# Performance work log

Measured on AMD Instinct MI355X. Metric: run time of the kernel, lower is better.

The kernel has to match this reference:

```python
import jax, jax.numpy as jnp
import numpy as np

NUM_NODE_TYPES = 8
HIDDEN = 64
D = 4
N_NODES = 100000
N_EDGES = 3200000
LN_EPS = 1e-5


def setup_inputs() -> dict:
    key = jax.random.key(0)
    ks = jax.random.split(key, 8)
    total_in = 2 * NUM_NODE_TYPES
    out_dim = D * D
    x = jax.random.normal(ks[0], (N_NODES, 16), dtype=jnp.float32)
    edge_index = jax.random.randint(ks[1], (2, N_EDGES), 0, N_NODES, dtype=jnp.int64)
    node_types = jax.random.randint(ks[2], (N_NODES,), 0, NUM_NODE_TYPES, dtype=jnp.int64)
    # LayerNorm params
    ln_g = jnp.ones((total_in,), dtype=jnp.float32)
    ln_b = jnp.zeros((total_in,), dtype=jnp.float32)
    # Linear layers (kaiming-ish init)
    W1 = jax.random.normal(ks[3], (total_in, HIDDEN), dtype=jnp.float32) * (1.0 / np.sqrt(total_in))
    b1 = jnp.zeros((HIDDEN,), dtype=jnp.float32)
    W2 = jax.random.normal(ks[4], (HIDDEN, out_dim), dtype=jnp.float32) * (1.0 / np.sqrt(HIDDEN))
    b2 = jnp.zeros((out_dim,), dtype=jnp.float32)
    return {"x": x, "edge_index": edge_index, "node_types": node_types,
            "ln_g": ln_g, "ln_b": ln_b, "W1": W1, "b1": b1, "W2": W2, "b2": b2}


def reference(x, edge_index, node_types, ln_g, ln_b, W1, b1, W2, b2):
    row, col = edge_index[0], edge_index[1]
    # one-hot node types then per-edge gather of src/tgt types
    onehot = jax.nn.one_hot(node_types, NUM_NODE_TYPES, dtype=jnp.float32)  # [N, T]
    h = jnp.concatenate([onehot[row], onehot[col]], axis=-1)  # [E, 2T]
    # LayerNorm
    mu = jnp.mean(h, axis=-1, keepdims=True)
    var = jnp.mean(jnp.square(h - mu), axis=-1, keepdims=True)
    hn = (h - mu) * jax.lax.rsqrt(var + LN_EPS) * ln_g + ln_b
    # MLP
    h1 = jax.nn.relu(hn @ W1 + b1)          # [E, HIDDEN]
    h_sheaf = (h1 @ W2 + b2).reshape(-1, D, D)  # [E, d, d]
    attention_maps = jax.nn.softmax(h_sheaf, axis=-1)
    sheaf_maps = jnp.eye(D, dtype=h_sheaf.dtype)[None] - attention_maps
    return sheaf_maps
```

## Files before the change

kernel.cpp:

```cpp
#include <hip/hip_runtime.h>
#include <math.h>

#define NUM_T   8
#define TIN     16
#define HID     64
#define OUTD    16
#define LN_EPS  1e-5f

typedef float f32x4 __attribute__((ext_vector_type(4)));

__global__ __launch_bounds__(256) void
build_table_kernel(const float* __restrict__ ln_g,
                   const float* __restrict__ ln_b,
                   const float* __restrict__ W1,
                   const float* __restrict__ b1,
                   const float* __restrict__ W2,
                   const float* __restrict__ b2,
                   f32x4* __restrict__ table4)
{
    __shared__ float sW1[TIN * HID];
    __shared__ float sW2[HID * OUTD];
    __shared__ float sb1[HID];
    __shared__ float sg[TIN], sb[TIN], sb2[OUTD];

    const int t = threadIdx.x;

    for (int i = t; i < TIN * HID; i += 256) sW1[i] = W1[i];
    for (int i = t; i < HID * OUTD; i += 256) sW2[i] = W2[i];
    if (t < HID) sb1[t] = b1[t];
    if (t < TIN) { sg[t] = ln_g[t]; sb[t] = ln_b[t]; }
    if (t < OUTD) sb2[t] = b2[t];
    __syncthreads();

    const int p  = t >> 2;
    const int kg = t & 3;
    const int ts = p >> 3;
    const int tt = p & 7;

    const float mu = 2.0f / 16.0f;
    float var = 0.0f;
    #pragma unroll
    for (int j = 0; j < TIN; ++j) {
        float h = (j == ts || j == (8 + tt)) ? 1.0f : 0.0f;
        float d = h - mu;
        var += d * d;
    }
    var *= (1.0f / 16.0f);
    const float inv = rsqrtf(var + LN_EPS);

    float hn[TIN];
    #pragma unroll
    for (int j = 0; j < TIN; ++j) {
        float h = (j == ts || j == (8 + tt)) ? 1.0f : 0.0f;
        hn[j] = (h - mu) * inv * sg[j] + sb[j];
    }

    float s[OUTD];
    #pragma unroll
    for (int o = 0; o < OUTD; ++o) s[o] = 0.0f;

    const int k0 = kg * 16;
    for (int k = k0; k < k0 + 16; ++k) {
        float a = sb1[k];
        #pragma unroll
        for (int j = 0; j < TIN; ++j) a += hn[j] * sW1[j * HID + k];
        a = fmaxf(a, 0.0f);
        #pragma unroll
        for (int o = 0; o < OUTD; ++o) s[o] += a * sW2[k * OUTD + o];
    }

    #pragma unroll
    for (int o = 0; o < OUTD; ++o) {
        s[o] += __shfl_xor(s[o], 1);
        s[o] += __shfl_xor(s[o], 2);
        s[o] += sb2[o];
    }

    const int r = kg;
    float s0 = s[4*r+0], s1 = s[4*r+1], s2 = s[4*r+2], s3 = s[4*r+3];
    float m  = fmaxf(fmaxf(s0, s1), fmaxf(s2, s3));
    float e0 = expf(s0 - m), e1 = expf(s1 - m),
          e2 = expf(s2 - m), e3 = expf(s3 - m);
    float rs = 1.0f / (e0 + e1 + e2 + e3);
    f32x4 outv;
    outv.x = (r == 0 ? 1.0f : 0.0f) - e0 * rs;
    outv.y = (r == 1 ? 1.0f : 0.0f) - e1 * rs;
    outv.z = (r == 2 ? 1.0f : 0.0f) - e2 * rs;
    outv.w = (r == 3 ? 1.0f : 0.0f) - e3 * rs;

    table4[t] = outv;
}

__global__ __launch_bounds__(256) void
scatter_edges_kernel(const int* __restrict__ row,
                     const int* __restrict__ col,
                     const int* __restrict__ ntypes,
                     const f32x4* __restrict__ table4,
                     f32x4* __restrict__ out4,
                     int E)
{
    __shared__ f32x4 lds_table[64 * 5];
    {
        int p = threadIdx.x >> 2, q = threadIdx.x & 3;
        lds_table[p * 5 + q] = table4[threadIdx.x];
    }
    __syncthreads();

    const int q      = threadIdx.x & 3;
    const int lane_e = threadIdx.x >> 2;
    const int stride = gridDim.x * 64;

    for (int e = blockIdx.x * 64 + lane_e; e < E; e += stride) {
        int r = row[e];
        int c = col[e];
        int pair = ntypes[r] * NUM_T + ntypes[c];
        f32x4 v = lds_table[pair * 5 + q];
        __builtin_nontemporal_store(v, &out4[e * 4 + q]);
    }
}

extern "C" void kernel_launch(void* const* d_in, const int* in_sizes, int n_in,
                              void* d_out, int out_size, void* d_ws, size_t ws_size,
                              hipStream_t stream)
{
    const int*   edge_index = (const int*)d_in[1];
    const int*   ntypes     = (const int*)d_in[2];
    const float* ln_g       = (const float*)d_in[3];
    const float* ln_b       = (const float*)d_in[4];
    const float* W1         = (const float*)d_in[5];
    const float* b1         = (const float*)d_in[6];
    const float* W2         = (const float*)d_in[7];
    const float* b2         = (const float*)d_in[8];

    const int E = in_sizes[1] / 2;

    f32x4* table4 = (f32x4*)d_ws;

    build_table_kernel<<<1, 256, 0, stream>>>(ln_g, ln_b, W1, b1, W2, b2, table4);

    const int blocks = 2048;
    scatter_edges_kernel<<<blocks, 256, 0, stream>>>(
        edge_index, edge_index + E, ntypes,
        table4, (f32x4*)d_out, E);
}
```

Before: 54.09 us.

## Fuse table build into edge kernel and load one index per lane with shuffles

Each of the 2048 blocks now computes the 64-entry sheaf-map table itself in shared memory, which removes the separate single-block launch and its global round trip. The edge loop also changes: each lane loads one edge's row, col and node types, and the pair ids are spread across lanes with wave shuffles. Before, four lanes loaded the same edge indices redundantly. The cost is that every block repeats the small MLP computation and loads the weights into shared memory before it can start scattering.

```diff
diff --git a/kernel.cpp b/kernel.cpp
--- a/kernel.cpp
+++ b/kernel.cpp
@@ -10,18 +10,23 @@
 typedef float f32x4 __attribute__((ext_vector_type(4)));
 
 __global__ __launch_bounds__(256) void
-build_table_kernel(const float* __restrict__ ln_g,
+fused_sheaf_kernel(const int* __restrict__ row,
+                   const int* __restrict__ col,
+                   const int* __restrict__ ntypes,
+                   const float* __restrict__ ln_g,
                    const float* __restrict__ ln_b,
                    const float* __restrict__ W1,
                    const float* __restrict__ b1,
                    const float* __restrict__ W2,
                    const float* __restrict__ b2,
-                   f32x4* __restrict__ table4)
+                   f32x4* __restrict__ out4,
+                   int E)
 {
     __shared__ float sW1[TIN * HID];
     __shared__ float sW2[HID * OUTD];
     __shared__ float sb1[HID];
     __shared__ float sg[TIN], sb[TIN], sb2[OUTD];
+    __shared__ f32x4 lds_table[64 * 5];
 
     const int t = threadIdx.x;
 
@@ -32,90 +37,89 @@
     if (t < OUTD) sb2[t] = b2[t];
     __syncthreads();
 
-    const int p  = t >> 2;
-    const int kg = t & 3;
-    const int ts = p >> 3;
-    const int tt = p & 7;
+    {
+        const int p  = t >> 2;
+        const int kg = t & 3;
+        const int ts = p >> 3;
+        const int tt = p & 7;
 
-    const float mu = 2.0f / 16.0f;
-    float var = 0.0f;
-    #pragma unroll
-    for (int j = 0; j < TIN; ++j) {
-        float h = (j == ts || j == (8 + tt)) ? 1.0f : 0.0f;
-        float d = h - mu;
-        var += d * d;
-    }
-    var *= (1.0f / 16.0f);
-    const float inv = rsqrtf(var + LN_EPS);
+        const float mu = 2.0f / 16.0f;
+        float var = 0.0f;
+        #pragma unroll
+        for (int j = 0; j < TIN; ++j) {
+            float h = (j == ts || j == (8 + tt)) ? 1.0f : 0.0f;
+            float d = h - mu;
+            var += d * d;
+        }
+        var *= (1.0f / 16.0f);
+        const float inv = rsqrtf(var + LN_EPS);
 
-    float hn[TIN];
-    #pragma unroll
-    for (int j = 0; j < TIN; ++j) {
-        float h = (j == ts || j == (8 + tt)) ? 1.0f : 0.0f;
-        hn[j] = (h - mu) * inv * sg[j] + sb[j];
-    }
+        float hn[TIN];
+        #pragma unroll
+        for (int j = 0; j < TIN; ++j) {
+            float h = (j == ts || j == (8 + tt)) ? 1.0f : 0.0f;
+            hn[j] = (h - mu) * inv * sg[j] + sb[j];
+        }
 
-    float s[OUTD];
-    #pragma unroll
-    for (int o = 0; o < OUTD; ++o) s[o] = 0.0f;
+        float s[OUTD];
+        #pragma unroll
+        for (int o = 0; o < OUTD; ++o) s[o] = 0.0f;
 
-    const int k0 = kg * 16;
-    for (int k = k0; k < k0 + 16; ++k) {
-        float a = sb1[k];
+        const int k0 = kg * 16;
+        for (int k = k0; k < k0 + 16; ++k) {
+            float a = sb1[k];
+            #pragma unroll
+            for (int j = 0; j < TIN; ++j) a += hn[j] * sW1[j * HID + k];
+            a = fmaxf(a, 0.0f);
+            #pragma unroll
+            for (int o = 0; o < OUTD; ++o) s[o] += a * sW2[k * OUTD + o];
+        }
+
         #pragma unroll
-        for (int j = 0; j < TIN; ++j) a += hn[j] * sW1[j * HID + k];
-        a = fmaxf(a, 0.0f);
-        #pragma unroll
-        for (int o = 0; o < OUTD; ++o) s[o] += a * sW2[k * OUTD + o];
-    }
+        for (int o = 0; o < OUTD; ++o) {
+            s[o] += __shfl_xor(s[o], 1);
+            s[o] += __shfl_xor(s[o], 2);
+            s[o] += sb2[o];
+        }
 
-    #pragma unroll
-    for (int o = 0; o < OUTD; ++o) {
-        s[o] += __shfl_xor(s[o], 1);
-        s[o] += __shfl_xor(s[o], 2);
-        s[o] += sb2[o];
-    }
-
-    const int r = kg;
-    float s0 = s[4*r+0], s1 = s[4*r+1], s2 = s[4*r+2], s3 = s[4*r+3];
-    float m  = fmaxf(fmaxf(s0, s1), fmaxf(s2, s3));
-    float e0 = expf(s0 - m), e1 = expf(s1 - m),
-          e2 = expf(s2 - m), e3 = expf(s3 - m);
-    float rs = 1.0f / (e0 + e1 + e2 + e3);
-    f32x4 outv;
-    outv.x = (r == 0 ? 1.0f : 0.0f) - e0 * rs;
-    outv.y = (r == 1 ? 1.0f : 0.0f) - e1 * rs;
-    outv.z = (r == 2 ? 1.0f : 0.0f) - e2 * rs;
-    outv.w = (r == 3 ? 1.0f : 0.0f) - e3 * rs;
-
-    table4[t] = outv;
-}
-
-__global__ __launch_bounds__(256) void
-scatter_edges_kernel(const int* __restrict__ row,
-                     const int* __restrict__ col,
-                     const int* __restrict__ ntypes,
-                     const f32x4* __restrict__ table4,
-                     f32x4* __restrict__ out4,
-                     int E)
-{
-    __shared__ f32x4 lds_table[64 * 5];
-    {
-        int p = threadIdx.x >> 2, q = threadIdx.x & 3;
-        lds_table[p * 5 + q] = table4[threadIdx.x];
+        const int r = kg;
+        float s0 = s[4*r+0], s1 = s[4*r+1], s2 = s[4*r+2], s3 = s[4*r+3];
+        float m  = fmaxf(fmaxf(s0, s1), fmaxf(s2, s3));
+        float e0 = expf(s0 - m), e1 = expf(s1 - m),
+              e2 = expf(s2 - m), e3 = expf(s3 - m);
+        float rs = 1.0f / (e0 + e1 + e2 + e3);
+        f32x4 outv;
+        outv.x = (r == 0 ? 1.0f : 0.0f) - e0 * rs;
+        outv.y = (r == 1 ? 1.0f : 0.0f) - e1 * rs;
+        outv.z = (r == 2 ? 1.0f : 0.0f) - e2 * rs;
+        outv.w = (r == 3 ? 1.0f : 0.0f) - e3 * rs;
+        lds_table[p * 5 + r] = outv;
     }
     __syncthreads();
 
-    const int q      = threadIdx.x & 3;
-    const int lane_e = threadIdx.x >> 2;
-    const int stride = gridDim.x * 64;
+    const int lane = t & 63;
+    const int wid  = t >> 6;
+    const int q    = lane & 3;
+    const int sub  = lane >> 2;
+    const int stride = gridDim.x * 256;
 
-    for (int e = blockIdx.x * 64 + lane_e; e < E; e += stride) {
-        int r = row[e];
-        int c = col[e];
+    for (int base = blockIdx.x * 256 + wid * 64; base < E; base += stride) {
+        int e  = base + lane;
+        int ec = (e < E) ? e : (E - 1);
+        int r = row[ec];
+        int c = col[ec];
         int pair = ntypes[r] * NUM_T + ntypes[c];
-        f32x4 v = lds_table[pair * 5 + q];
-        __builtin_nontemporal_store(v, &out4[e * 4 + q]);
+
+        #pragma unroll
+        for (int j = 0; j < 4; ++j) {
+            int src = j * 16 + sub;
+            int pj  = __shfl(pair, src, 64);
+            int ej  = base + src;
+            if (ej < E) {
+                f32x4 v = lds_table[pj * 5 + q];
+                __builtin_nontemporal_store(v, &out4[ej * 4 + q]);
+            }
+        }
     }
 }
 
@@ -134,12 +138,9 @@
 
     const int E = in_sizes[1] / 2;
 
-    f32x4* table4 = (f32x4*)d_ws;
-
-    build_table_kernel<<<1, 256, 0, stream>>>(ln_g, ln_b, W1, b1, W2, b2, table4);
-
     const int blocks = 2048;
-    scatter_edges_kernel<<<blocks, 256, 0, stream>>>(
+    fused_sheaf_kernel<<<blocks, 256, 0, stream>>>(
         edge_index, edge_index + E, ntypes,
-        table4, (f32x4*)d_out, E);
+        ln_g, ln_b, W1, b1, W2, b2,
+        (f32x4*)d_out, E);
 }
```

After: 58.82 us. 1.09x slower.

## Pack node types into 4-bit LDS array and drop global type gathers

Applied to the files above, without the earlier changes.

A prep kernel now packs the node types as 4-bit entries, eight per 32-bit word (about 50KB), alongside building the 64-pair lookup table. Each scatter block copies the whole packed array into LDS, so the per-edge type lookups become LDS reads instead of random global gathers. The scatter grid shrinks to 512 blocks to spread the per-block cost of staging that array. The size is hardcoded to 100000 nodes (N_PACK_U32 = 12500), the large LDS footprint limits occupancy, and larger node counts would read past the end of the packed array.

```diff
diff --git a/kernel.cpp b/kernel.cpp
--- a/kernel.cpp
+++ b/kernel.cpp
@@ -7,23 +7,42 @@
 #define OUTD    16
 #define LN_EPS  1e-5f
 
+#define N_PACK_U32 12500
+
 typedef float f32x4 __attribute__((ext_vector_type(4)));
 
 __global__ __launch_bounds__(256) void
-build_table_kernel(const float* __restrict__ ln_g,
-                   const float* __restrict__ ln_b,
-                   const float* __restrict__ W1,
-                   const float* __restrict__ b1,
-                   const float* __restrict__ W2,
-                   const float* __restrict__ b2,
-                   f32x4* __restrict__ table4)
+prep_kernel(const int* __restrict__ ntypes, int n_nodes,
+            const float* __restrict__ ln_g,
+            const float* __restrict__ ln_b,
+            const float* __restrict__ W1,
+            const float* __restrict__ b1,
+            const float* __restrict__ W2,
+            const float* __restrict__ b2,
+            f32x4* __restrict__ table4,
+            unsigned int* __restrict__ packed)
 {
+    const int t = threadIdx.x;
+    const int g = blockIdx.x * 256 + t;
+
+    if (g < N_PACK_U32) {
+        unsigned int w = 0;
+        int n0 = g * 8;
+        #pragma unroll
+        for (int j = 0; j < 8; ++j) {
+            int n = n0 + j;
+            unsigned int ty = (n < n_nodes) ? (unsigned int)ntypes[n] : 0u;
+            w |= (ty & 7u) << (j * 4);
+        }
+        packed[g] = w;
+    }
+
+    if (blockIdx.x != 0) return;
+
     __shared__ float sW1[TIN * HID];
     __shared__ float sW2[HID * OUTD];
     __shared__ float sb1[HID];
     __shared__ float sg[TIN], sb[TIN], sb2[OUTD];
-
-    const int t = threadIdx.x;
 
     for (int i = t; i < TIN * HID; i += 256) sW1[i] = W1[i];
     for (int i = t; i < HID * OUTD; i += 256) sW2[i] = W2[i];
@@ -87,33 +106,47 @@
     outv.y = (r == 1 ? 1.0f : 0.0f) - e1 * rs;
     outv.z = (r == 2 ? 1.0f : 0.0f) - e2 * rs;
     outv.w = (r == 3 ? 1.0f : 0.0f) - e3 * rs;
-
-    table4[t] = outv;
+    table4[p * 4 + r] = outv;
 }
 
 __global__ __launch_bounds__(256) void
 scatter_edges_kernel(const int* __restrict__ row,
                      const int* __restrict__ col,
-                     const int* __restrict__ ntypes,
+                     const unsigned int* __restrict__ packed,
                      const f32x4* __restrict__ table4,
                      f32x4* __restrict__ out4,
                      int E)
 {
     __shared__ f32x4 lds_table[64 * 5];
+    __shared__ unsigned int nt_lds[N_PACK_U32];
+
+    const int t = threadIdx.x;
+
     {
-        int p = threadIdx.x >> 2, q = threadIdx.x & 3;
-        lds_table[p * 5 + q] = table4[threadIdx.x];
+        int p = t >> 2, q = t & 3;
+        lds_table[p * 5 + q] = table4[t];
+    }
+    {
+        const uint4* src4 = (const uint4*)packed;
+        uint4* dst4 = (uint4*)nt_lds;
+        for (int i = t; i < N_PACK_U32 / 4; i += 256) dst4[i] = src4[i];
+        for (int i = (N_PACK_U32 & ~3) + t; i < N_PACK_U32; i += 256)
+            nt_lds[i] = packed[i];
     }
     __syncthreads();
 
-    const int q      = threadIdx.x & 3;
-    const int lane_e = threadIdx.x >> 2;
+    const int q      = t & 3;
+    const int lane_e = t >> 2;
     const int stride = gridDim.x * 64;
 
     for (int e = blockIdx.x * 64 + lane_e; e < E; e += stride) {
         int r = row[e];
         int c = col[e];
-        int pair = ntypes[r] * NUM_T + ntypes[c];
+        unsigned int wr = nt_lds[r >> 3];
+        unsigned int wc = nt_lds[c >> 3];
+        int tr = (wr >> ((r & 7) * 4)) & 7;
+        int tc = (wc >> ((c & 7) * 4)) & 7;
+        int pair = (tr << 3) | tc;
         f32x4 v = lds_table[pair * 5 + q];
         __builtin_nontemporal_store(v, &out4[e * 4 + q]);
     }
@@ -133,13 +166,17 @@
     const float* b2         = (const float*)d_in[8];
 
     const int E = in_sizes[1] / 2;
+    const int N = in_sizes[2];
 
-    f32x4* table4 = (f32x4*)d_ws;
+    f32x4*        table4 = (f32x4*)d_ws;
+    unsigned int* packed = (unsigned int*)((char*)d_ws + 4096);
 
-    build_table_kernel<<<1, 256, 0, stream>>>(ln_g, ln_b, W1, b1, W2, b2, table4);
+    const int prep_blocks = (N_PACK_U32 + 255) / 256;
+    prep_kernel<<<prep_blocks, 256, 0, stream>>>(
+        ntypes, N, ln_g, ln_b, W1, b1, W2, b2, table4, packed);
 
-    const int blocks = 2048;
+    const int blocks = 512;
     scatter_edges_kernel<<<blocks, 256, 0, stream>>>(
-        edge_index, edge_index + E, ntypes,
+        edge_index, edge_index + E, packed,
         table4, (f32x4*)d_out, E);
 }
```

After: 53.71 us. No clear change (-0.7%).
